# Optimization experiments

Hardware: AMD Instinct MI355X
Metric: run time of the kernel (lower is better)

Reference implementation:

```python
import jax, jax.numpy as jnp
import numpy as np
from jax import lax

B, C, L, K = 16, 128, 16000, 256
STRIDE = 4
ITERS = 10
DT, TAU = 0.01, 0.1
THR = 0.5


def setup_inputs() -> dict:
    key = jax.random.key(0)
    k1, k2 = jax.random.split(key)
    mini_batch = jax.random.normal(k1, (B, 1, L), dtype=jnp.float32)
    # dictionary / filterbank weights (stand-in for cm.compute_weights())
    weights = jax.random.normal(k2, (C, 1, K), dtype=jnp.float32) / np.sqrt(K).astype(np.float32)
    return {"mini_batch": mini_batch, "weights": weights}


def _conv1d(x, w, stride):
    # x: [B, Cin, L], w: [Cout, Cin, K] -> [B, Cout, S]  (torch F.conv1d, VALID)
    return lax.conv_general_dilated(
        x, w, window_strides=(stride,), padding="VALID",
        dimension_numbers=("NCH", "OIH", "NCH"))


def _conv_transpose1d(a, w, stride):
    # a: [B, C, S], w: [C, 1, K] -> [B, 1, (S-1)*stride + K]  (torch F.conv_transpose1d)
    k = w.shape[-1]
    w_t = jnp.flip(jnp.swapaxes(w, 0, 1), -1)  # [1, C, K]
    return lax.conv_general_dilated(
        a, w_t, window_strides=(1,), padding=[(k - 1, k - 1)],
        lhs_dilation=(stride,), dimension_numbers=("NCH", "OIH", "NCH"))


def _hard_shrink(u, thr):
    return jnp.where(jnp.abs(u) > thr, u, jnp.zeros((), u.dtype))


def reference(mini_batch, weights):
    # LCA fixed-point dynamics:
    #   u <- u + dt/tau * (W*x - u - W*(W^T a) + a),  a = HardShrink(u, thr)
    step_size = jnp.float32(DT / TAU)
    drive = _conv1d(mini_batch, weights, STRIDE)  # [B, C, S] precomputed driver
    u0 = jnp.zeros_like(drive)

    def step(u, _):
        a = _hard_shrink(u, THR)
        recon = _conv_transpose1d(a, weights, STRIDE)      # [B, 1, L]
        feedback = _conv1d(recon, weights, STRIDE)          # [B, C, S]
        u_new = u + step_size * (drive - u - feedback + a)
        return u_new, None

    u, _ = lax.scan(step, u0, None, length=ITERS)
    a = _hard_shrink(u, THR)  # spikegram / sparse code
    return a
```

## Files before the change

### kernel.cpp

```cpp
#include <hip/hip_runtime.h>
#include <math.h>

#define BB 16
#define CC 128
#define LL 16000
#define KK 256
#define SS 3937
#define MM 4000
#define THRS 0.5f
#define STEP 0.1f

template<int MODE>
__global__ __launch_bounds__(256, 2) void k_conv(
    const float* __restrict__ in0,
    const float* __restrict__ W,
    float* __restrict__ drive,
    float* __restrict__ u)
{
    __shared__ __align__(16) float sW[2][128 * 68];
    __shared__ __align__(16) float sX[768];
    __shared__ int sFlag;

    const int tid = threadIdx.x;
    const int tx = tid & 15;
    const int ty = tid >> 4;
    const int s0 = blockIdx.x * 128;
    const int b  = blockIdx.y;

    const int sc = tid >> 1;
    const int sg = (tid & 1) * 8;
    const float4* W4 = (const float4*)W;

    if (tid == 0) sFlag = 0;
    __syncthreads();

    bool nz = false;
    #pragma unroll
    for (int h = 0; h < 3; ++h) {
        int t = tid + 256 * h;
        int l = 4 * s0 + t;
        float v = (l < LL) ? in0[b * LL + l] : 0.f;
        sX[t] = v;
        nz |= (v != 0.f);
    }
    if (MODE != 0) { if (nz) atomicOr(&sFlag, 1); }
    __syncthreads();

    float acc[8][8];
    #pragma unroll
    for (int i = 0; i < 8; ++i)
        #pragma unroll
        for (int j = 0; j < 8; ++j) acc[i][j] = 0.f;

    const bool doit = (MODE == 0) || (sFlag != 0);

    if (doit) {
        {
            float4* dst = (float4*)sW[0];
            #pragma unroll
            for (int w = 0; w < 8; ++w)
                dst[sc * 17 + sg + w] = W4[sc * 64 + sg + w];
        }
        __syncthreads();

        for (int kc = 0; kc < 4; ++kc) {
            float4 pre[8];
            if (kc < 3) {
                #pragma unroll
                for (int w = 0; w < 8; ++w)
                    pre[w] = W4[sc * 64 + (kc + 1) * 16 + sg + w];
            }

            const float* wbuf = sW[kc & 1];
            const int xoff = 64 * kc;

            for (int kk4 = 0; kk4 < 16; ++kk4) {
                float4 xq[8];
                #pragma unroll
                for (int j = 0; j < 8; ++j)
                    xq[j] = *(const float4*)&sX[4 * (tx + 16 * j) + xoff + 4 * kk4];
                float4 w4[8];
                #pragma unroll
                for (int i = 0; i < 8; ++i)
                    w4[i] = *(const float4*)&wbuf[(ty + 16 * i) * 68 + 4 * kk4];
                #pragma unroll
                for (int dk = 0; dk < 4; ++dk) {
                    #pragma unroll
                    for (int i = 0; i < 8; ++i) {
                        float wv = (&w4[i].x)[dk];
                        #pragma unroll
                        for (int j = 0; j < 8; ++j)
                            acc[i][j] = fmaf(wv, (&xq[j].x)[dk], acc[i][j]);
                    }
                }
            }

            if (kc < 3) {
                float4* dst = (float4*)sW[(kc + 1) & 1];
                #pragma unroll
                for (int w = 0; w < 8; ++w)
                    dst[sc * 17 + sg + w] = pre[w];
            }
            __syncthreads();
        }
    }

    #pragma unroll
    for (int j = 0; j < 8; ++j) {
        int s = s0 + tx + 16 * j;
        if (s < SS) {
            #pragma unroll
            for (int i = 0; i < 8; ++i) {
                int c = ty + 16 * i;
                size_t idx = (size_t)(b * CC + c) * SS + s;
                if (MODE == 0) {
                    float d = acc[i][j];
                    drive[idx] = d;
                    u[idx] = __fmul_rn(STEP, d);
                } else {
                    float uo = u[idx];
                    float dr = drive[idx];
                    float a  = (fabsf(uo) > THRS) ? uo : 0.f;
                    float t1 = __fsub_rn(dr, uo);
                    float t2 = __fsub_rn(t1, acc[i][j]);
                    float t3 = __fadd_rn(t2, a);
                    float t4 = __fmul_rn(STEP, t3);
                    float un = __fadd_rn(uo, t4);
                    if (MODE == 1) u[idx] = un;
                    else           u[idx] = (fabsf(un) > THRS) ? un : 0.f;
                }
            }
        }
    }
}

#define FMAC_DPP(ACC, WREG, AREG, QI) \
    asm("v_fmac_f32_dpp %0, %1, %2 row_newbcast:" #QI " row_mask:0xf bank_mask:0xf" \
        : "+v"(ACC) : "v"(WREG), "v"(AREG))

#define QSTEP2(WQ, QB, QI) { \
    float a_ = arow[16 * (QB) + (QI)]; \
    FMAC_DPP(accA, WQ.x, a_, QI); \
    FMAC_DPP(accB, WQ.y, a_, QI); }

#define QBLOCK2(WQ, QB) \
    QSTEP2(WQ, QB, 0)  QSTEP2(WQ, QB, 1)  QSTEP2(WQ, QB, 2)  QSTEP2(WQ, QB, 3)  \
    QSTEP2(WQ, QB, 4)  QSTEP2(WQ, QB, 5)  QSTEP2(WQ, QB, 6)  QSTEP2(WQ, QB, 7)  \
    QSTEP2(WQ, QB, 8)  QSTEP2(WQ, QB, 9)  QSTEP2(WQ, QB, 10) QSTEP2(WQ, QB, 11) \
    QSTEP2(WQ, QB, 12) QSTEP2(WQ, QB, 13) QSTEP2(WQ, QB, 14) QSTEP2(WQ, QB, 15)

__global__ __launch_bounds__(512, 1) void k_recon(
    const float* __restrict__ u,
    const float* __restrict__ W,
    float* __restrict__ recon)
{
    __shared__ __align__(16) float sA[2][32 * 320];
    __shared__ int sFlag;

    const int tid  = threadIdx.x;
    const int p    = tid & 15;
    const int ml   = tid & 255;
    const int rp   = (tid >> 8) << 1;
    const int m0 = blockIdx.x * 256;
    const int b  = blockIdx.y;
    const int m  = m0 + ml;

    if (tid == 0) sFlag = 0;
    __syncthreads();

    float accA = 0.f, accB = 0.f;

    const float* Wq0 = W + 4 * (63 - p)      + rp;
    const float* Wq1 = W + 4 * (63 - 16 - p) + rp;
    const float* Wq2 = W + 4 * (63 - 32 - p) + rp;
    const float* Wq3 = W + 4 * (63 - 48 - p) + rp;

    {
        bool nz = false;
        #pragma unroll
        for (int h = 0; h < 20; ++h) {
            int idx = tid + 512 * h;
            int cl  = idx / 320;
            int col = idx - cl * 320;
            int mm  = m0 - 63 + col;
            float v = 0.f;
            if (col < 319 && mm >= 0 && mm < SS) {
                float uu = u[(size_t)(b * CC + cl) * SS + mm];
                v = (fabsf(uu) > THRS) ? uu : 0.f;
            }
            sA[0][idx] = v;
            nz |= (v != 0.f);
        }
        if (nz) atomicOr(&sFlag, 1);
    }

    for (int cs = 0; cs < 4; ++cs) {
        const int c0 = cs * 32;

        __syncthreads();
        const int f = (sFlag >> cs) & 1;

        float pv[20];
        if (cs < 3) {
            const int c0n = (cs + 1) * 32;
            #pragma unroll
            for (int h = 0; h < 20; ++h) {
                int idx = tid + 512 * h;
                int cl  = idx / 320;
                int col = idx - cl * 320;
                int mm  = m0 - 63 + col;
                float v = 0.f;
                if (col < 319 && mm >= 0 && mm < SS)
                    v = u[(size_t)(b * CC + c0n + cl) * SS + mm];
                pv[h] = v;
            }
        }

        if (f) {
            const float* buf = sA[cs & 1];
            size_t co = (size_t)c0 * KK;
            float2 w0 = *(const float2*)(Wq0 + co);
            float2 w1 = *(const float2*)(Wq1 + co);
            float2 w2 = *(const float2*)(Wq2 + co);
            float2 w3 = *(const float2*)(Wq3 + co);

            for (int cl = 0; cl < 32; ++cl) {
                float2 n0, n1, n2, n3;
                if (cl < 31) {
                    size_t cn = (size_t)(c0 + cl + 1) * KK;
                    n0 = *(const float2*)(Wq0 + cn);
                    n1 = *(const float2*)(Wq1 + cn);
                    n2 = *(const float2*)(Wq2 + cn);
                    n3 = *(const float2*)(Wq3 + cn);
                }

                const float* arow = buf + cl * 320 + ml;
                QBLOCK2(w0, 0)
                QBLOCK2(w1, 1)
                QBLOCK2(w2, 2)
                QBLOCK2(w3, 3)

                w0 = n0; w1 = n1; w2 = n2; w3 = n3;
            }
        }

        if (cs < 3) {
            bool nz = false;
            float* dst = sA[(cs + 1) & 1];
            #pragma unroll
            for (int h = 0; h < 20; ++h) {
                int idx = tid + 512 * h;
                float uu = pv[h];
                float v = (fabsf(uu) > THRS) ? uu : 0.f;
                dst[idx] = v;
                nz |= (v != 0.f);
            }
            if (nz) atomicOr(&sFlag, 1 << (cs + 1));
        }
    }

    if (m < MM) {
        float2* o = (float2*)(recon + (size_t)b * LL + 4 * m + rp);
        *o = make_float2(accA, accB);
    }
}

extern "C" void kernel_launch(void* const* d_in, const int* in_sizes, int n_in,
                              void* d_out, int out_size, void* d_ws, size_t ws_size,
                              hipStream_t stream) {
    const float* x = (const float*)d_in[0];
    const float* W = (const float*)d_in[1];
    float* u = (float*)d_out;

    float* ws    = (float*)d_ws;
    float* drive = ws;
    float* recon = drive + (size_t)BB * CC * SS;

    dim3 gConv(31, 16);
    k_conv<0><<<gConv, 256, 0, stream>>>(x, W, drive, u);

    for (int it = 0; it < 9; ++it) {
        k_recon<<<dim3(16, 16), 512, 0, stream>>>(u, W, recon);
        if (it < 8)
            k_conv<1><<<gConv, 256, 0, stream>>>(recon, W, drive, u);
        else
            k_conv<2><<<gConv, 256, 0, stream>>>(recon, W, drive, u);
    }
}
```

Before: 1.703 ms.

## Store u in padded aligned layout and split recon reads between LDS and global

Stores u in a workspace buffer with row stride 4064 and a 64-element leading pad, so recon can read it with aligned, bounds-free indexing. The recon kernel then takes half of its activation operands directly from global memory (shrink applied inline) and the other half from LDS, to relieve LDS bandwidth in the inner DPP FMA loop. The cost is an extra zeroing kernel, more global and L2 traffic in the hot loop, and a fallback to the old path when the workspace is too small.

```diff
diff --git a/kernel.cpp b/kernel.cpp
--- a/kernel.cpp
+++ b/kernel.cpp
@@ -7,15 +7,23 @@
 #define KK 256
 #define SS 3937
 #define MM 4000
+#define UST 4064
 #define THRS 0.5f
 #define STEP 0.1f
 
-template<int MODE>
+__global__ void k_zero(float4* p, int n4) {
+    int i = blockIdx.x * blockDim.x + threadIdx.x;
+    int stride = gridDim.x * blockDim.x;
+    for (; i < n4; i += stride) p[i] = make_float4(0.f, 0.f, 0.f, 0.f);
+}
+
+template<int MODE, int PAD>
 __global__ __launch_bounds__(256, 2) void k_conv(
     const float* __restrict__ in0,
     const float* __restrict__ W,
     float* __restrict__ drive,
-    float* __restrict__ u)
+    float* __restrict__ u,
+    float* __restrict__ out)
 {
     __shared__ __align__(16) float sW[2][128 * 68];
     __shared__ __align__(16) float sX[768];
@@ -112,13 +120,14 @@
             #pragma unroll
             for (int i = 0; i < 8; ++i) {
                 int c = ty + 16 * i;
-                size_t idx = (size_t)(b * CC + c) * SS + s;
+                size_t idx  = (size_t)(b * CC + c) * SS + s;
+                size_t idxu = PAD ? ((size_t)(b * CC + c) * UST + 64 + s) : idx;
                 if (MODE == 0) {
                     float d = acc[i][j];
                     drive[idx] = d;
-                    u[idx] = __fmul_rn(STEP, d);
+                    u[idxu] = __fmul_rn(STEP, d);
                 } else {
-                    float uo = u[idx];
+                    float uo = u[idxu];
                     float dr = drive[idx];
                     float a  = (fabsf(uo) > THRS) ? uo : 0.f;
                     float t1 = __fsub_rn(dr, uo);
@@ -126,8 +135,8 @@
                     float t3 = __fadd_rn(t2, a);
                     float t4 = __fmul_rn(STEP, t3);
                     float un = __fadd_rn(uo, t4);
-                    if (MODE == 1) u[idx] = un;
-                    else           u[idx] = (fabsf(un) > THRS) ? un : 0.f;
+                    if (MODE == 1) u[idxu] = un;
+                    else           out[idx] = (fabsf(un) > THRS) ? un : 0.f;
                 }
             }
         }
@@ -140,6 +149,12 @@
 
 #define QSTEP2(WQ, QB, QI) { \
     float a_ = arow[16 * (QB) + (QI)]; \
+    FMAC_DPP(accA, WQ.x, a_, QI); \
+    FMAC_DPP(accB, WQ.y, a_, QI); }
+
+#define QSTEP2G(WQ, QB, QI) { \
+    float uu_ = grow[16 * (QB) + (QI)]; \
+    float a_ = (fabsf(uu_) > THRS) ? uu_ : 0.f; \
     FMAC_DPP(accA, WQ.x, a_, QI); \
     FMAC_DPP(accB, WQ.y, a_, QI); }
 
@@ -149,7 +164,130 @@
     QSTEP2(WQ, QB, 8)  QSTEP2(WQ, QB, 9)  QSTEP2(WQ, QB, 10) QSTEP2(WQ, QB, 11) \
     QSTEP2(WQ, QB, 12) QSTEP2(WQ, QB, 13) QSTEP2(WQ, QB, 14) QSTEP2(WQ, QB, 15)
 
-__global__ __launch_bounds__(512, 1) void k_recon(
+#define QBLOCK2S(WQ, QB) \
+    QSTEP2(WQ, QB, 0)  QSTEP2G(WQ, QB, 1)  QSTEP2(WQ, QB, 2)  QSTEP2G(WQ, QB, 3)  \
+    QSTEP2(WQ, QB, 4)  QSTEP2G(WQ, QB, 5)  QSTEP2(WQ, QB, 6)  QSTEP2G(WQ, QB, 7)  \
+    QSTEP2(WQ, QB, 8)  QSTEP2G(WQ, QB, 9)  QSTEP2(WQ, QB, 10) QSTEP2G(WQ, QB, 11) \
+    QSTEP2(WQ, QB, 12) QSTEP2G(WQ, QB, 13) QSTEP2(WQ, QB, 14) QSTEP2G(WQ, QB, 15)
+
+__global__ __launch_bounds__(512, 1) void k_recon_sp(
+    const float* __restrict__ up,
+    const float* __restrict__ W,
+    float* __restrict__ recon)
+{
+    __shared__ __align__(16) float sA[2][32 * 320];
+    __shared__ int sFlag;
+
+    const int tid  = threadIdx.x;
+    const int p    = tid & 15;
+    const int ml   = tid & 255;
+    const int rp   = (tid >> 8) << 1;
+    const int m0 = blockIdx.x * 256;
+    const int b  = blockIdx.y;
+    const int m  = m0 + ml;
+
+    if (tid == 0) sFlag = 0;
+    __syncthreads();
+
+    float accA = 0.f, accB = 0.f;
+
+    const float* Wq0 = W + 4 * (63 - p)      + rp;
+    const float* Wq1 = W + 4 * (63 - 16 - p) + rp;
+    const float* Wq2 = W + 4 * (63 - 32 - p) + rp;
+    const float* Wq3 = W + 4 * (63 - 48 - p) + rp;
+
+    const float* gub = up + (size_t)b * CC * UST + (m0 + 1) + ml;
+
+    {
+        bool nz = false;
+        #pragma unroll
+        for (int h = 0; h < 20; ++h) {
+            int idx = tid + 512 * h;
+            int cl  = idx / 320;
+            int col = idx - cl * 320;
+            float v = 0.f;
+            if (col < 319) {
+                float uu = up[(size_t)(b * CC + cl) * UST + (m0 + 1) + col];
+                v = (fabsf(uu) > THRS) ? uu : 0.f;
+            }
+            sA[0][idx] = v;
+            nz |= (v != 0.f);
+        }
+        if (nz) atomicOr(&sFlag, 1);
+    }
+
+    for (int cs = 0; cs < 4; ++cs) {
+        const int c0 = cs * 32;
+
+        __syncthreads();
+        const int f = (sFlag >> cs) & 1;
+
+        float pv[20];
+        if (cs < 3) {
+            const int c0n = (cs + 1) * 32;
+            #pragma unroll
+            for (int h = 0; h < 20; ++h) {
+                int idx = tid + 512 * h;
+                int cl  = idx / 320;
+                int col = idx - cl * 320;
+                float v = 0.f;
+                if (col < 319)
+                    v = up[(size_t)(b * CC + c0n + cl) * UST + (m0 + 1) + col];
+                pv[h] = v;
+            }
+        }
+
+        if (f) {
+            const float* buf = sA[cs & 1];
+            size_t co = (size_t)c0 * KK;
+            float2 w0 = *(const float2*)(Wq0 + co);
+            float2 w1 = *(const float2*)(Wq1 + co);
+            float2 w2 = *(const float2*)(Wq2 + co);
+            float2 w3 = *(const float2*)(Wq3 + co);
+
+            for (int cl = 0; cl < 32; ++cl) {
+                float2 n0, n1, n2, n3;
+                if (cl < 31) {
+                    size_t cn = (size_t)(c0 + cl + 1) * KK;
+                    n0 = *(const float2*)(Wq0 + cn);
+                    n1 = *(const float2*)(Wq1 + cn);
+                    n2 = *(const float2*)(Wq2 + cn);
+                    n3 = *(const float2*)(Wq3 + cn);
+                }
+
+                const float* arow = buf + cl * 320 + ml;
+                const float* grow = gub + (size_t)(c0 + cl) * UST;
+                QBLOCK2S(w0, 0)
+                QBLOCK2S(w1, 1)
+                QBLOCK2S(w2, 2)
+                QBLOCK2S(w3, 3)
+
+                w0 = n0; w1 = n1; w2 = n2; w3 = n3;
+            }
+        }
+
+        if (cs < 3) {
+            bool nz = false;
+            float* dst = sA[(cs + 1) & 1];
+            #pragma unroll
+            for (int h = 0; h < 20; ++h) {
+                int idx = tid + 512 * h;
+                float uu = pv[h];
+                float v = (fabsf(uu) > THRS) ? uu : 0.f;
+                dst[idx] = v;
+                nz |= (v != 0.f);
+            }
+            if (nz) atomicOr(&sFlag, 1 << (cs + 1));
+        }
+    }
+
+    if (m < MM) {
+        float2* o = (float2*)(recon + (size_t)b * LL + 4 * m + rp);
+        *o = make_float2(accA, accB);
+    }
+}
+
+__global__ __launch_bounds__(512, 1) void k_recon_base(
     const float* __restrict__ u,
     const float* __restrict__ W,
     float* __restrict__ recon)
@@ -270,20 +408,36 @@
                               hipStream_t stream) {
     const float* x = (const float*)d_in[0];
     const float* W = (const float*)d_in[1];
-    float* u = (float*)d_out;
 
     float* ws    = (float*)d_ws;
     float* drive = ws;
     float* recon = drive + (size_t)BB * CC * SS;
+    float* upad  = recon + (size_t)BB * LL;
+
+    const size_t upad_f = (size_t)(BB * CC + 1) * UST;
+    const size_t need = ((size_t)BB * CC * SS + (size_t)BB * LL + upad_f) * 4;
 
     dim3 gConv(31, 16);
-    k_conv<0><<<gConv, 256, 0, stream>>>(x, W, drive, u);
-
-    for (int it = 0; it < 9; ++it) {
-        k_recon<<<dim3(16, 16), 512, 0, stream>>>(u, W, recon);
-        if (it < 8)
-            k_conv<1><<<gConv, 256, 0, stream>>>(recon, W, drive, u);
-        else
-            k_conv<2><<<gConv, 256, 0, stream>>>(recon, W, drive, u);
+
+    if (ws_size >= need) {
+        k_zero<<<1024, 256, 0, stream>>>((float4*)upad, (int)(upad_f / 4));
+        k_conv<0, 1><<<gConv, 256, 0, stream>>>(x, W, drive, upad, (float*)d_out);
+        for (int it = 0; it < 9; ++it) {
+            k_recon_sp<<<dim3(16, 16), 512, 0, stream>>>(upad, W, recon);
+            if (it < 8)
+                k_conv<1, 1><<<gConv, 256, 0, stream>>>(recon, W, drive, upad, (float*)d_out);
+            else
+                k_conv<2, 1><<<gConv, 256, 0, stream>>>(recon, W, drive, upad, (float*)d_out);
+        }
+    } else {
+        float* u = (float*)d_out;
+        k_conv<0, 0><<<gConv, 256, 0, stream>>>(x, W, drive, u, u);
+        for (int it = 0; it < 9; ++it) {
+            k_recon_base<<<dim3(16, 16), 512, 0, stream>>>(u, W, recon);
+            if (it < 8)
+                k_conv<1, 0><<<gConv, 256, 0, stream>>>(recon, W, drive, u, u);
+            else
+                k_conv<2, 0><<<gConv, 256, 0, stream>>>(recon, W, drive, u, u);
+        }
     }
 }
```

New measurement: 2.003 ms. 17.6% more time.
